# Kernel tuning notes

Measured on AMD Instinct MI355X. Metric: run time of the kernel, lower is better.

## Reference

```python
import jax, jax.numpy as jnp
import numpy as np

N_NODES = 50000
N_EDGES = 1600000
IN_DIM = 128
HEADS = 2
OUT_CH = 32
NEG_SLOPE = 0.2


def setup_inputs() -> dict:
    key = jax.random.key(0)
    k1, k2, k3, k4, k5, k6 = jax.random.split(key, 6)
    x = jax.random.normal(k1, (N_NODES, IN_DIM), dtype=jnp.float32)
    # Glorot-ish scale for weights
    W = jax.random.normal(k2, (IN_DIM, HEADS * OUT_CH), dtype=jnp.float32) * (1.0 / np.sqrt(IN_DIM))
    att_src = jax.random.normal(k3, (HEADS, OUT_CH), dtype=jnp.float32) * (1.0 / np.sqrt(OUT_CH))
    att_dst = jax.random.normal(k4, (HEADS, OUT_CH), dtype=jnp.float32) * (1.0 / np.sqrt(OUT_CH))
    bias = jnp.zeros((HEADS * OUT_CH,), dtype=jnp.float32)
    edge_index = jax.random.randint(k5, (2, N_EDGES), 0, N_NODES, dtype=jnp.int32)
    return {"x": x, "W": W, "att_src": att_src, "att_dst": att_dst,
            "bias": bias, "edge_index": edge_index}


def reference(x, W, att_src, att_dst, bias, edge_index):
    N = x.shape[0]
    # ELU on input features (IntraGraphAttention.forward)
    xf = jax.nn.elu(x)
    # Shared linear projection, per-head view: [N, H, C]
    h = (xf @ W).reshape(N, HEADS, OUT_CH)
    # add_self_loops=True (PyG GATConv default)
    loops = jnp.arange(N, dtype=edge_index.dtype)
    src = jnp.concatenate([edge_index[0], loops])
    dst = jnp.concatenate([edge_index[1], loops])
    # Per-node attention halves: [N, H]
    a_src = jnp.einsum('nhc,hc->nh', h, att_src)
    a_dst = jnp.einsum('nhc,hc->nh', h, att_dst)
    # Per-edge logits with leaky relu: [E, H]
    logits = a_src[src] + a_dst[dst]
    logits = jnp.where(logits >= 0, logits, NEG_SLOPE * logits)
    # Segment softmax over incoming edges of each dst node
    seg_max = jax.ops.segment_max(logits, dst, num_segments=N)
    e = jnp.exp(logits - seg_max[dst])
    denom = jax.ops.segment_sum(e, dst, num_segments=N)
    alpha = e / (denom[dst] + 1e-16)  # [E, H]
    # Weighted scatter-aggregate of source features: [N, H, C]
    msgs = h[src] * alpha[:, :, None]
    out = jax.ops.segment_sum(msgs, dst, num_segments=N)
    # concat=True -> [N, H*C], plus bias
    return out.reshape(N, HEADS * OUT_CH) + bias
```

## Files before the change

### kernel.cpp

```cpp
#include <hip/hip_runtime.h>
#include <hip/hip_bf16.h>

#define NN 50000
#define EE 1600000
#define PROJ_BLOCKS 1563
#define SRC_SPLIT 25000

using short8 = __attribute__((ext_vector_type(8))) short;
using float4v = __attribute__((ext_vector_type(4))) float;

__device__ __forceinline__ float bflo(unsigned u) { return __uint_as_float(u << 16); }
__device__ __forceinline__ float bfhi(unsigned u) { return __uint_as_float(u & 0xffff0000u); }
__device__ __forceinline__ unsigned short f2bf(float v) {
  return __bfloat16_as_ushort(__float2bfloat16(v));
}

__global__ __launch_bounds__(256) void k_pre(
    const float* __restrict__ x, const float* __restrict__ W,
    const float* __restrict__ att_src, const float* __restrict__ att_dst,
    float2* __restrict__ a_src2, float2* __restrict__ a_dst2,
    int* __restrict__ head8, unsigned short* __restrict__ wt16, int nblocks) {
  __shared__ float wa_s[128][2], wa_d[128][2];
  int tid = threadIdx.x;
  {
    int k = tid >> 1, hh = tid & 1;
    const float* wrow = W + k * 64 + hh * 32;
    const float* as = att_src + hh * 32;
    const float* ad = att_dst + hh * 32;
    float ss = 0.f, dd = 0.f;
#pragma unroll 8
    for (int c = 0; c < 32; ++c) { float wv = wrow[c]; ss += wv * as[c]; dd += wv * ad[c]; }
    wa_s[k][hh] = ss; wa_d[k][hh] = dd;
  }
  if (blockIdx.x < 32) {
    int i = blockIdx.x * 256 + tid;
    int k = i >> 6, n = i & 63;
    wt16[n * 128 + k] = f2bf(W[i]);
  }
  int gsize = nblocks * 256;
  for (int i = blockIdx.x * 256 + tid; i < NN * 8; i += gsize) head8[i] = -1;
  __syncthreads();

  int w = tid >> 6, lane = tid & 63;
  int g = lane >> 4, q = lane & 15;
  int k0 = q * 8;
  float ws0[8], ws1[8], wd0[8], wd1[8];
#pragma unroll
  for (int j = 0; j < 8; ++j) {
    ws0[j] = wa_s[k0 + j][0]; ws1[j] = wa_s[k0 + j][1];
    wd0[j] = wa_d[k0 + j][0]; wd1[j] = wa_d[k0 + j][1];
  }
  int stride = nblocks * 16;
  for (int n = blockIdx.x * 16 + w * 4 + g; n < NN; n += stride) {
    float4 xa = *(const float4*)&x[n * 128 + k0];
    float4 xb = *(const float4*)&x[n * 128 + k0 + 4];
    float v[8] = {xa.x, xa.y, xa.z, xa.w, xb.x, xb.y, xb.z, xb.w};
    float s0 = 0.f, s1 = 0.f, d0 = 0.f, d1 = 0.f;
#pragma unroll
    for (int j = 0; j < 8; ++j) {
      float e = v[j] > 0.f ? v[j] : __expf(v[j]) - 1.f;
      s0 += e * ws0[j]; s1 += e * ws1[j];
      d0 += e * wd0[j]; d1 += e * wd1[j];
    }
#pragma unroll
    for (int o = 8; o > 0; o >>= 1) {
      s0 += __shfl_xor(s0, o); s1 += __shfl_xor(s1, o);
      d0 += __shfl_xor(d0, o); d1 += __shfl_xor(d1, o);
    }
    if (q == 0) { a_src2[n] = make_float2(s0, s1); a_dst2[n] = make_float2(d0, d1); }
  }
}

__global__ __launch_bounds__(256) void k_mid(
    const float* __restrict__ x, const unsigned short* __restrict__ wt16,
    const int* __restrict__ src, const int* __restrict__ dst,
    const float2* __restrict__ a_src2, const float2* __restrict__ a_dst2,
    int* __restrict__ head8, int4* __restrict__ edge4, unsigned* __restrict__ h2u) {
  int bid = blockIdx.x;
  int tid = threadIdx.x;
  if (bid >= PROJ_BLOCKS) {
    int ea = (bid - PROJ_BLOCKS) * 512 + tid;
    int eb = ea + 256;
    int sa = src[ea], da = dst[ea];
    int sb = src[eb], db = dst[eb];
    float2 asa = a_src2[sa], ada = a_dst2[da];
    float2 asb = a_src2[sb], adb = a_dst2[db];
    float la0 = asa.x + ada.x; la0 = fmaxf(la0, 0.2f * la0);
    float la1 = asa.y + ada.y; la1 = fmaxf(la1, 0.2f * la1);
    float lb0 = asb.x + adb.x; lb0 = fmaxf(lb0, 0.2f * lb0);
    float lb1 = asb.y + adb.y; lb1 = fmaxf(lb1, 0.2f * lb1);
    int ca = ((sa >= SRC_SPLIT) ? 4 : 0) + (ea & 3);
    int cb = ((sb >= SRC_SPLIT) ? 4 : 0) + (eb & 3);
    int olda = atomicExch(&head8[da * 8 + ca], ea);
    int oldb = atomicExch(&head8[db * 8 + cb], eb);
    edge4[ea] = make_int4(sa, olda, __float_as_int(__expf(la0)), __float_as_int(__expf(la1)));
    edge4[eb] = make_int4(sb, oldb, __float_as_int(__expf(lb0)), __float_as_int(__expf(lb1)));
    return;
  }
  __shared__ unsigned short Wt[64 * 136];
  __shared__ unsigned short xs[32 * 136];
  int row0 = bid * 32;
#pragma unroll
  for (int it = 0; it < 4; ++it) {
    int idx = it * 2048 + tid * 8;
    int n = idx >> 7, k = idx & 127;
    *(short8*)&Wt[n * 136 + k] = *(const short8*)&wt16[idx];
  }
  for (int i = tid; i < 2048; i += 256) {
    int r = i >> 6, k2 = (i & 63) * 2;
    int row = row0 + r;
    float v0 = 0.f, v1 = 0.f;
    if (row < NN) { float2 xv = *(const float2*)&x[row * 128 + k2]; v0 = xv.x; v1 = xv.y; }
    v0 = v0 > 0.f ? v0 : __expf(v0) - 1.f;
    v1 = v1 > 0.f ? v1 : __expf(v1) - 1.f;
    *(unsigned*)&xs[r * 136 + k2] = (unsigned)f2bf(v0) | ((unsigned)f2bf(v1) << 16);
  }
  __syncthreads();
  int w = tid >> 6, lane = tid & 63;
  int t = w >> 1, ch = w & 1;
  int m = lane & 15, quad = lane >> 4;
  float4v acc[2] = {{0, 0, 0, 0}, {0, 0, 0, 0}};
#pragma unroll
  for (int ks = 0; ks < 4; ++ks) {
    int koff = quad * 8 + ks * 32;
    short8 af = *(const short8*)&xs[(t * 16 + m) * 136 + koff];
#pragma unroll
    for (int j = 0; j < 2; ++j) {
      int nt = ch * 2 + j;
      short8 bf = *(const short8*)&Wt[(nt * 16 + m) * 136 + koff];
      acc[j] = __builtin_amdgcn_mfma_f32_16x16x32_bf16(af, bf, acc[j], 0, 0, 0);
    }
  }
#pragma unroll
  for (int j = 0; j < 2; ++j) {
    int nt = ch * 2 + j;
#pragma unroll
    for (int reg = 0; reg < 4; ++reg) {
      float v = acc[j][reg];
      float vhi = __shfl_xor(v, 1);
      int row = row0 + t * 16 + quad * 4 + reg;
      if (!(m & 1) && row < NN) {
        h2u[row * 32 + nt * 8 + (m >> 1)] =
            (unsigned)f2bf(v) | ((unsigned)f2bf(vhi) << 16);
      }
    }
  }
}

__global__ __launch_bounds__(256) void k_agg(
    const unsigned* __restrict__ h2u, const float2* __restrict__ a_src2,
    const float2* __restrict__ a_dst2, const int4* __restrict__ head8v,
    const int4* __restrict__ edge4, const float* __restrict__ bias,
    float* __restrict__ out) {
  int lane = threadIdx.x & 63;
  int half = lane >> 5;
  int n = blockIdx.x * 8 + (threadIdx.x >> 6) * 2 + half;
  int c2 = lane & 31;
  int hh = c2 >> 4;

  float denom, acc0, acc1;
  {
    float2 as = a_src2[n], ad = a_dst2[n];
    float l0 = (hh ? as.y + ad.y : as.x + ad.x);
    l0 = fmaxf(l0, 0.2f * l0);
    float es = __expf(l0);
    unsigned hv = h2u[n * 32 + c2];
    denom = es; acc0 = es * bflo(hv); acc1 = es * bfhi(hv);
  }

  int4 hdA = head8v[n * 2];
  int4 hdB = head8v[n * 2 + 1];
#pragma unroll
  for (int ph = 0; ph < 2; ++ph) {
    int4 hd = ph ? hdB : hdA;
    int e0 = hd.x, e1 = hd.y, e2 = hd.z, e3 = hd.w;
    while (max(max(e0, e1), max(e2, e3)) >= 0) {
      int4 p0 = edge4[max(e0, 0)];
      int4 p1 = edge4[max(e1, 0)];
      int4 p2 = edge4[max(e2, 0)];
      int4 p3 = edge4[max(e3, 0)];
      unsigned h0 = h2u[p0.x * 32 + c2], h1 = h2u[p1.x * 32 + c2];
      unsigned h2 = h2u[p2.x * 32 + c2], h3 = h2u[p3.x * 32 + c2];
      float x0 = (e0 >= 0) ? __int_as_float(hh ? p0.w : p0.z) : 0.f;
      float x1 = (e1 >= 0) ? __int_as_float(hh ? p1.w : p1.z) : 0.f;
      float x2 = (e2 >= 0) ? __int_as_float(hh ? p2.w : p2.z) : 0.f;
      float x3 = (e3 >= 0) ? __int_as_float(hh ? p3.w : p3.z) : 0.f;
      denom += (x0 + x1) + (x2 + x3);
      acc0 += x0 * bflo(h0) + x1 * bflo(h1) + x2 * bflo(h2) + x3 * bflo(h3);
      acc1 += x0 * bfhi(h0) + x1 * bfhi(h1) + x2 * bfhi(h2) + x3 * bfhi(h3);
      e0 = (e0 >= 0) ? p0.y : -1;
      e1 = (e1 >= 0) ? p1.y : -1;
      e2 = (e2 >= 0) ? p2.y : -1;
      e3 = (e3 >= 0) ? p3.y : -1;
    }
  }
  float inv = 1.f / (denom + 1e-16f);
  float2 b = ((const float2*)bias)[c2];
  ((float2*)out)[n * 32 + c2] = make_float2(acc0 * inv + b.x, acc1 * inv + b.y);
}

extern "C" void kernel_launch(void* const* d_in, const int* in_sizes, int n_in,
                              void* d_out, int out_size, void* d_ws, size_t ws_size,
                              hipStream_t stream) {
  const float* x       = (const float*)d_in[0];
  const float* W       = (const float*)d_in[1];
  const float* att_src = (const float*)d_in[2];
  const float* att_dst = (const float*)d_in[3];
  const float* bias    = (const float*)d_in[4];
  const int* edge_index = (const int*)d_in[5];
  const int* esrc = edge_index;
  const int* edst = edge_index + EE;

  char* base = (char*)d_ws;
  unsigned* h2u  = (unsigned*)base;
  float2* a_src2 = (float2*)(base + 6400000);
  float2* a_dst2 = (float2*)(base + 6800000);
  int*    head8  = (int*)(base + 7200000);
  int4*   edge4  = (int4*)(base + 8800000);
  unsigned short* wt16 = (unsigned short*)d_out;

  const int PRE_BLOCKS = 1024;
  k_pre<<<PRE_BLOCKS, 256, 0, stream>>>(x, W, att_src, att_dst, a_src2, a_dst2,
                                        head8, wt16, PRE_BLOCKS);
  k_mid<<<PROJ_BLOCKS + EE / 512, 256, 0, stream>>>(x, wt16, esrc, edst, a_src2,
                                                    a_dst2, head8, edge4, h2u);
  k_agg<<<NN / 8, 256, 0, stream>>>(h2u, a_src2, a_dst2, (const int4*)head8,
                                    edge4, bias, (float*)d_out);
}
```

Measured before the change: 227.8 us.

## Replace per-dst linked lists with fixed-slot slabs plus overflow chain

Edges are now bucketed by destination into a fixed 32-slot slab per node through an atomic counter, and extra edges spill into a linked-list overflow area. Attention weights are stored packed as two bf16 values in 8-byte entries instead of 16-byte linked-list nodes. Aggregation streams contiguous slab entries with vector loads, which removes the dependent pointer-chasing latency of the old lists. The cost is lower precision in the edge weights and extra contention from atomicAdd on the per-node counter.

Result: slower. 301.2 us (+32.2%).

```diff
diff --git a/kernel.cpp b/kernel.cpp
--- a/kernel.cpp
+++ b/kernel.cpp
@@ -4,7 +4,8 @@
 #define NN 50000
 #define EE 1600000
 #define PROJ_BLOCKS 1563
-#define SRC_SPLIT 25000
+#define SLOTS 32
+#define OVF_CAP 262144
 
 using short8 = __attribute__((ext_vector_type(8))) short;
 using float4v = __attribute__((ext_vector_type(4))) float;
@@ -19,7 +20,8 @@
     const float* __restrict__ x, const float* __restrict__ W,
     const float* __restrict__ att_src, const float* __restrict__ att_dst,
     float2* __restrict__ a_src2, float2* __restrict__ a_dst2,
-    int* __restrict__ head8, unsigned short* __restrict__ wt16, int nblocks) {
+    int* __restrict__ cnt, int* __restrict__ head1, int* __restrict__ ovf_cur,
+    unsigned short* __restrict__ wt16, int nblocks) {
   __shared__ float wa_s[128][2], wa_d[128][2];
   int tid = threadIdx.x;
   {
@@ -37,8 +39,9 @@
     int k = i >> 6, n = i & 63;
     wt16[n * 128 + k] = f2bf(W[i]);
   }
+  if (blockIdx.x == 0 && tid == 0) *ovf_cur = 0;
   int gsize = nblocks * 256;
-  for (int i = blockIdx.x * 256 + tid; i < NN * 8; i += gsize) head8[i] = -1;
+  for (int i = blockIdx.x * 256 + tid; i < NN; i += gsize) { cnt[i] = 0; head1[i] = -1; }
   __syncthreads();
 
   int w = tid >> 6, lane = tid & 63;
@@ -75,26 +78,39 @@
     const float* __restrict__ x, const unsigned short* __restrict__ wt16,
     const int* __restrict__ src, const int* __restrict__ dst,
     const float2* __restrict__ a_src2, const float2* __restrict__ a_dst2,
-    int* __restrict__ head8, int4* __restrict__ edge4, unsigned* __restrict__ h2u) {
+    int* __restrict__ cnt, int* __restrict__ head1, int* __restrict__ ovf_cur,
+    int2* __restrict__ slab, int4* __restrict__ ovf, unsigned* __restrict__ h2u) {
   int bid = blockIdx.x;
   int tid = threadIdx.x;
   if (bid >= PROJ_BLOCKS) {
     int ea = (bid - PROJ_BLOCKS) * 512 + tid;
     int eb = ea + 256;
     int sa = src[ea], da = dst[ea];
-    int sb = src[eb], db = dst[eb];
+    int sbn = src[eb], db = dst[eb];
     float2 asa = a_src2[sa], ada = a_dst2[da];
-    float2 asb = a_src2[sb], adb = a_dst2[db];
+    float2 asb = a_src2[sbn], adb = a_dst2[db];
     float la0 = asa.x + ada.x; la0 = fmaxf(la0, 0.2f * la0);
     float la1 = asa.y + ada.y; la1 = fmaxf(la1, 0.2f * la1);
     float lb0 = asb.x + adb.x; lb0 = fmaxf(lb0, 0.2f * lb0);
     float lb1 = asb.y + adb.y; lb1 = fmaxf(lb1, 0.2f * lb1);
-    int ca = ((sa >= SRC_SPLIT) ? 4 : 0) + (ea & 3);
-    int cb = ((sb >= SRC_SPLIT) ? 4 : 0) + (eb & 3);
-    int olda = atomicExch(&head8[da * 8 + ca], ea);
-    int oldb = atomicExch(&head8[db * 8 + cb], eb);
-    edge4[ea] = make_int4(sa, olda, __float_as_int(__expf(la0)), __float_as_int(__expf(la1)));
-    edge4[eb] = make_int4(sb, oldb, __float_as_int(__expf(lb0)), __float_as_int(__expf(lb1)));
+    unsigned wa = (unsigned)f2bf(__expf(la0)) | ((unsigned)f2bf(__expf(la1)) << 16);
+    unsigned wb = (unsigned)f2bf(__expf(lb0)) | ((unsigned)f2bf(__expf(lb1)) << 16);
+    int pa = atomicAdd(&cnt[da], 1);
+    if (pa < SLOTS) {
+      slab[da * SLOTS + pa] = make_int2(sa, (int)wa);
+    } else {
+      int op = atomicAdd(ovf_cur, 1);
+      int old = atomicExch(&head1[da], op);
+      ovf[op] = make_int4(sa, old, (int)wa, 0);
+    }
+    int pb = atomicAdd(&cnt[db], 1);
+    if (pb < SLOTS) {
+      slab[db * SLOTS + pb] = make_int2(sbn, (int)wb);
+    } else {
+      int op = atomicAdd(ovf_cur, 1);
+      int old = atomicExch(&head1[db], op);
+      ovf[op] = make_int4(sbn, old, (int)wb, 0);
+    }
     return;
   }
   __shared__ unsigned short Wt[64 * 136];
@@ -149,8 +165,9 @@
 
 __global__ __launch_bounds__(256) void k_agg(
     const unsigned* __restrict__ h2u, const float2* __restrict__ a_src2,
-    const float2* __restrict__ a_dst2, const int4* __restrict__ head8v,
-    const int4* __restrict__ edge4, const float* __restrict__ bias,
+    const float2* __restrict__ a_dst2, const int* __restrict__ cnt,
+    const int* __restrict__ head1, const int2* __restrict__ slab,
+    const int4* __restrict__ ovf, const float* __restrict__ bias,
     float* __restrict__ out) {
   int lane = threadIdx.x & 63;
   int half = lane >> 5;
@@ -168,32 +185,41 @@
     denom = es; acc0 = es * bflo(hv); acc1 = es * bfhi(hv);
   }
 
-  int4 hdA = head8v[n * 2];
-  int4 hdB = head8v[n * 2 + 1];
-#pragma unroll
-  for (int ph = 0; ph < 2; ++ph) {
-    int4 hd = ph ? hdB : hdA;
-    int e0 = hd.x, e1 = hd.y, e2 = hd.z, e3 = hd.w;
-    while (max(max(e0, e1), max(e2, e3)) >= 0) {
-      int4 p0 = edge4[max(e0, 0)];
-      int4 p1 = edge4[max(e1, 0)];
-      int4 p2 = edge4[max(e2, 0)];
-      int4 p3 = edge4[max(e3, 0)];
-      unsigned h0 = h2u[p0.x * 32 + c2], h1 = h2u[p1.x * 32 + c2];
-      unsigned h2 = h2u[p2.x * 32 + c2], h3 = h2u[p3.x * 32 + c2];
-      float x0 = (e0 >= 0) ? __int_as_float(hh ? p0.w : p0.z) : 0.f;
-      float x1 = (e1 >= 0) ? __int_as_float(hh ? p1.w : p1.z) : 0.f;
-      float x2 = (e2 >= 0) ? __int_as_float(hh ? p2.w : p2.z) : 0.f;
-      float x3 = (e3 >= 0) ? __int_as_float(hh ? p3.w : p3.z) : 0.f;
-      denom += (x0 + x1) + (x2 + x3);
-      acc0 += x0 * bflo(h0) + x1 * bflo(h1) + x2 * bflo(h2) + x3 * bflo(h3);
-      acc1 += x0 * bfhi(h0) + x1 * bfhi(h1) + x2 * bfhi(h2) + x3 * bfhi(h3);
-      e0 = (e0 >= 0) ? p0.y : -1;
-      e1 = (e1 >= 0) ? p1.y : -1;
-      e2 = (e2 >= 0) ? p2.y : -1;
-      e3 = (e3 >= 0) ? p3.y : -1;
-    }
-  }
+  int cv = cnt[n];
+  int m32 = cv < SLOTS ? cv : SLOTS;
+  const int4* sb4 = (const int4*)(slab + (long)n * SLOTS);
+  for (int j = 0; j < m32; j += 4) {
+    int4 ra = sb4[j >> 1];
+    int4 rb = sb4[(j >> 1) + 1];
+    bool v1 = (j + 1 < m32), v2 = (j + 2 < m32), v3 = (j + 3 < m32);
+    int i0 = ra.x;
+    int i1 = v1 ? ra.z : i0;
+    int i2 = v2 ? rb.x : i0;
+    int i3 = v3 ? rb.z : i0;
+    unsigned h0 = h2u[i0 * 32 + c2], h1 = h2u[i1 * 32 + c2];
+    unsigned h2 = h2u[i2 * 32 + c2], h3 = h2u[i3 * 32 + c2];
+    unsigned w0p = (unsigned)ra.y, w1p = (unsigned)ra.w;
+    unsigned w2p = (unsigned)rb.y, w3p = (unsigned)rb.w;
+    float x0 = hh ? bfhi(w0p) : bflo(w0p);
+    float x1 = v1 ? (hh ? bfhi(w1p) : bflo(w1p)) : 0.f;
+    float x2 = v2 ? (hh ? bfhi(w2p) : bflo(w2p)) : 0.f;
+    float x3 = v3 ? (hh ? bfhi(w3p) : bflo(w3p)) : 0.f;
+    denom += (x0 + x1) + (x2 + x3);
+    acc0 += x0 * bflo(h0) + x1 * bflo(h1) + x2 * bflo(h2) + x3 * bflo(h3);
+    acc1 += x0 * bfhi(h0) + x1 * bfhi(h1) + x2 * bfhi(h2) + x3 * bfhi(h3);
+  }
+  int e = head1[n];
+  while (e >= 0) {
+    int4 p = ovf[e];
+    unsigned hv = h2u[p.x * 32 + c2];
+    unsigned wp = (unsigned)p.z;
+    float xw = hh ? bfhi(wp) : bflo(wp);
+    denom += xw;
+    acc0 += xw * bflo(hv);
+    acc1 += xw * bfhi(hv);
+    e = p.y;
+  }
+
   float inv = 1.f / (denom + 1e-16f);
   float2 b = ((const float2*)bias)[c2];
   ((float2*)out)[n * 32 + c2] = make_float2(acc0 * inv + b.x, acc1 * inv + b.y);
@@ -212,18 +238,22 @@
   const int* edst = edge_index + EE;
 
   char* base = (char*)d_ws;
-  unsigned* h2u  = (unsigned*)base;
-  float2* a_src2 = (float2*)(base + 6400000);
-  float2* a_dst2 = (float2*)(base + 6800000);
-  int*    head8  = (int*)(base + 7200000);
-  int4*   edge4  = (int4*)(base + 8800000);
+  unsigned* h2u   = (unsigned*)base;
+  float2* a_src2  = (float2*)(base + 6400000);
+  float2* a_dst2  = (float2*)(base + 6800000);
+  int*    cnt     = (int*)(base + 7200000);
+  int*    head1   = (int*)(base + 7400000);
+  int*    ovf_cur = (int*)(base + 7600000);
+  int2*   slab    = (int2*)(base + 7680000);
+  int4*   ovf     = (int4*)(base + 20480000);
   unsigned short* wt16 = (unsigned short*)d_out;
 
   const int PRE_BLOCKS = 1024;
   k_pre<<<PRE_BLOCKS, 256, 0, stream>>>(x, W, att_src, att_dst, a_src2, a_dst2,
-                                        head8, wt16, PRE_BLOCKS);
+                                        cnt, head1, ovf_cur, wt16, PRE_BLOCKS);
   k_mid<<<PROJ_BLOCKS + EE / 512, 256, 0, stream>>>(x, wt16, esrc, edst, a_src2,
-                                                    a_dst2, head8, edge4, h2u);
-  k_agg<<<NN / 8, 256, 0, stream>>>(h2u, a_src2, a_dst2, (const int4*)head8,
-                                    edge4, bias, (float*)d_out);
-}
+                                                    a_dst2, cnt, head1, ovf_cur,
+                                                    slab, ovf, h2u);
+  k_agg<<<NN / 8, 256, 0, stream>>>(h2u, a_src2, a_dst2, cnt, head1, slab, ovf,
+                                    bias, (float*)d_out);
+}
```
